# Kernel optimization log

Hardware: AMD Instinct MI355X
Metric: run time of the kernel (lower is better)

## Reference

```python
import jax, jax.numpy as jnp
import numpy as np

N_OR = 8          # orientations of the SE(2) discretization
BN_EPS = 1e-5


def _rotate_kernel(W, theta):
    """Rotate a spatial kernel [..., k, k] about its center by theta.
    Bilinear interpolation, zeros outside the kernel support."""
    k = W.shape[-1]
    c = (k - 1) / 2.0
    ys, xs = jnp.meshgrid(jnp.arange(k, dtype=jnp.float32) - c,
                          jnp.arange(k, dtype=jnp.float32) - c, indexing="ij")
    cos, sin = jnp.cos(theta), jnp.sin(theta)
    sy = cos * ys - sin * xs + c   # source coords: rotate sample grid by -theta
    sx = sin * ys + cos * xs + c
    y0 = jnp.floor(sy).astype(jnp.int32)
    x0 = jnp.floor(sx).astype(jnp.int32)
    wy = (sy - y0).astype(W.dtype)
    wx = (sx - x0).astype(W.dtype)

    def gather(yi, xi):
        valid = ((yi >= 0) & (yi < k) & (xi >= 0) & (xi < k)).astype(W.dtype)
        yc = jnp.clip(yi, 0, k - 1)
        xc = jnp.clip(xi, 0, k - 1)
        return W[..., yc, xc] * valid

    return (gather(y0, x0) * (1 - wy) * (1 - wx)
            + gather(y0, x0 + 1) * (1 - wy) * wx
            + gather(y0 + 1, x0) * wy * (1 - wx)
            + gather(y0 + 1, x0 + 1) * wy * wx)


def _thetas():
    return 2.0 * jnp.pi * jnp.arange(N_OR, dtype=jnp.float32) / N_OR


def _lift(x, W):
    """LiftM2Cartesian. x: [B,Cin,H,W] (pre-padded), W: [Cout,Cin,k,k].
    Returns [B,Cout,8,H',W']."""
    Wr = jax.vmap(lambda t: _rotate_kernel(W, t))(_thetas())  # [8,Cout,Cin,k,k]
    co = W.shape[0]
    Wf = Wr.reshape((N_OR * co,) + W.shape[1:])
    y = jax.lax.conv_general_dilated(x, Wf, (1, 1), "VALID",
                                     dimension_numbers=("NCHW", "OIHW", "NCHW"))
    B, _, H, Wd = y.shape
    return y.reshape(B, N_OR, co, H, Wd).transpose(0, 2, 1, 3, 4)


def _gconv(x, K):
    """ConvM2Cartesian. x: [B,Cin,8,H,W] (spatially pre-padded),
    K: [Cout,Cin,8,k,k]. Output orientation m uses the kernel spatially
    rotated by theta_m with the orientation axis cyclically shifted by m."""
    cout, cin, _, k, _ = K.shape
    # orient_idx[m, o] = (o - m) mod 8
    orient_idx = (jnp.arange(N_OR)[None, :] - jnp.arange(N_OR)[:, None]) % N_OR
    Kshift = jnp.moveaxis(K[:, :, orient_idx], 2, 0)        # [8m,Cout,Cin,8o,k,k]
    Km = jax.vmap(_rotate_kernel)(Kshift, _thetas())         # [8m,Cout,Cin,8o,k,k]
    Kf = Km.reshape(N_OR * cout, cin * N_OR, k, k)
    B, _, _, H, Wd = x.shape
    xf = x.reshape(B, cin * N_OR, H, Wd)
    y = jax.lax.conv_general_dilated(xf, Kf, (1, 1), "VALID",
                                     dimension_numbers=("NCHW", "OIHW", "NCHW"))
    Ho, Wo = y.shape[-2:]
    return y.reshape(B, N_OR, cout, Ho, Wo).transpose(0, 2, 1, 3, 4)


def _bn3d(x, gamma, beta):
    """BatchNorm3d (training-mode batch statistics). x: [B,C,O,H,W]."""
    mean = jnp.mean(x, axis=(0, 2, 3, 4), keepdims=True)
    var = jnp.mean((x - mean) ** 2, axis=(0, 2, 3, 4), keepdims=True)
    g = gamma.reshape(1, -1, 1, 1, 1)
    b = beta.reshape(1, -1, 1, 1, 1)
    return g * (x - mean) * jax.lax.rsqrt(var + BN_EPS) + b


def _pad_m2(x, p):
    return jnp.pad(x, ((0, 0), (0, 0), (0, 0), (p, p), (p, p)), mode="reflect")


def setup_inputs() -> dict:
    key = jax.random.key(0)
    ks = jax.random.split(key, 8)
    c = 16
    cin = 3
    x = jax.random.normal(ks[0], (2, cin, 256, 256), dtype=jnp.float32)
    lift_w = jax.random.normal(ks[1], (c, cin, 7, 7), dtype=jnp.float32) / np.sqrt(cin * 49)
    w1 = jax.random.normal(ks[2], (c, c, N_OR, 5, 5), dtype=jnp.float32) / np.sqrt(c * N_OR * 25)
    w2 = jax.random.normal(ks[3], (c, c, N_OR, 5, 5), dtype=jnp.float32) / np.sqrt(c * N_OR * 25)
    w3 = jax.random.normal(ks[4], (c, c, N_OR, 5, 5), dtype=jnp.float32) / np.sqrt(c * N_OR * 25)
    w4 = jax.random.normal(ks[5], (c, c, N_OR, 1, 1), dtype=jnp.float32) / np.sqrt(c * N_OR)
    final_w = jax.random.normal(ks[6], (1, c), dtype=jnp.float32) / np.sqrt(c)
    ones = jnp.ones((c,), dtype=jnp.float32)
    zeros = jnp.zeros((c,), dtype=jnp.float32)
    return {"x": x, "lift_w": lift_w, "w1": w1, "w2": w2, "w3": w3, "w4": w4,
            "final_w": final_w,
            "g0": ones, "b0": zeros, "g1": ones, "b1": zeros, "g2": ones,
            "b2": zeros, "g3": ones, "b3": zeros, "g4": ones, "b4": zeros}


def reference(x, lift_w, w1, w2, w3, w4, final_w,
              g0, b0, g1, b1, g2, b2, g3, b3, g4, b4):
    # lift: ReflectionPad2d(3) -> LiftM2Cartesian(7) -> BN3d -> ReLU
    xp = jnp.pad(x, ((0, 0), (0, 0), (3, 3), (3, 3)), mode="reflect")
    h = jax.nn.relu(_bn3d(_lift(xp, lift_w), g0, b0))          # [B,16,8,H,W]
    # conv1..3: ReflectionPadM2(2) -> ConvM2Cartesian(5) -> BN3d -> ReLU (Dropout3d is identity in eval)
    h = jax.nn.relu(_bn3d(_gconv(_pad_m2(h, 2), w1), g1, b1))
    h = jax.nn.relu(_bn3d(_gconv(_pad_m2(h, 2), w2), g2, b2))
    h = jax.nn.relu(_bn3d(_gconv(_pad_m2(h, 2), w3), g3, b3))
    # conv4: 1x1 group conv -> BN3d -> ReLU
    h = jax.nn.relu(_bn3d(_gconv(h, w4), g4, b4))
    # MaxProjectM2: max over orientation axis
    h = jnp.max(h, axis=2)                                     # [B,16,H,W]
    # final 1x1 conv (no bias) + sigmoid
    return jax.nn.sigmoid(jnp.einsum("bchw,oc->bohw", h, final_w))
```

## Files before the change

### kernel.cpp

```cpp
#include <hip/hip_runtime.h>
#include <hip/hip_bf16.h>
#include <math.h>

#define HW 65536
#define WID 256
#define NOR 8
#define PLANE_C (NOR * HW)
#define PLANE_B (16 * NOR * HW)
#define BN_N 1048576.0f
#define NHWC_STRIDE 136

typedef __attribute__((ext_vector_type(8)))  short  short8;
typedef __attribute__((ext_vector_type(4)))  short  short4v;
typedef __attribute__((ext_vector_type(16))) float  float16;
typedef __attribute__((ext_vector_type(4)))  float  float4v;

__device__ __forceinline__ float b2f(short s) {
    union { unsigned int u; float f; } c;
    c.u = ((unsigned int)(unsigned short)s) << 16;
    return c.f;
}
__device__ __forceinline__ short f2b(float f) {
    union { __hip_bfloat16 h; short s; } c;
    c.h = __float2bfloat16(f);
    return c.s;
}
__device__ __forceinline__ float ldv(const void* p, int i, int isbf) {
    return isbf ? b2f(((const short*)p)[i]) : ((const float*)p)[i];
}

__global__ void detect_cvt_k(const void* x, const void* fw,
                             const void* g0, const void* b0, const void* g1, const void* b1,
                             const void* g2, const void* b2, const void* g3, const void* b3,
                             const void* g4, const void* b4,
                             float* __restrict__ gbF, float* __restrict__ fwF,
                             int* __restrict__ flag) {
    __shared__ int bad;
    if (threadIdx.x == 0) bad = 0;
    __syncthreads();
    const __hip_bfloat16* p = (const __hip_bfloat16*)x;
    for (int i = threadIdx.x; i < 4096; i += 256) {
        float v = __bfloat162float(p[i]);
        if (!(fabsf(v) < 1e4f)) atomicOr(&bad, 1);
    }
    __syncthreads();
    int isbf = bad ? 0 : 1;
    if (threadIdx.x == 0) *flag = isbf;
    int t = threadIdx.x;
    if (t < 160) {
        const void* srcs[10] = {g0, b0, g1, b1, g2, b2, g3, b3, g4, b4};
        gbF[t] = ldv(srcs[t >> 4], t & 15, isbf);
    } else if (t < 176) {
        fwF[t - 160] = ldv(fw, t - 160, isbf);
    }
}

__device__ float rot_sample_g(const void* __restrict__ W, int isbf, int k, float theta,
                              int i, int j) {
    float c = 0.5f * (float)(k - 1);
    float ys = (float)i - c, xs = (float)j - c;
    float cs = cosf(theta), sn = sinf(theta);
    float sy = cs * ys - sn * xs + c;
    float sx = sn * ys + cs * xs + c;
    float fy = floorf(sy), fx = floorf(sx);
    int y0 = (int)fy, x0 = (int)fx;
    float wy = sy - fy, wx = sx - fx;
    float v00 = (y0 >= 0 && y0 < k && x0 >= 0 && x0 < k)                 ? ldv(W, y0 * k + x0, isbf)           : 0.f;
    float v01 = (y0 >= 0 && y0 < k && x0 + 1 >= 0 && x0 + 1 < k)         ? ldv(W, y0 * k + x0 + 1, isbf)       : 0.f;
    float v10 = (y0 + 1 >= 0 && y0 + 1 < k && x0 >= 0 && x0 < k)         ? ldv(W, (y0 + 1) * k + x0, isbf)     : 0.f;
    float v11 = (y0 + 1 >= 0 && y0 + 1 < k && x0 + 1 >= 0 && x0 + 1 < k) ? ldv(W, (y0 + 1) * k + x0 + 1, isbf) : 0.f;
    return v00 * (1 - wy) * (1 - wx) + v01 * (1 - wy) * wx
         + v10 * wy * (1 - wx) + v11 * wy * wx;
}

__device__ __forceinline__ float theta_of(int m) {
    return (6.2831855f * (float)m) / 8.0f;
}

__device__ __forceinline__ int mirror(int i) {
    i = i < 0 ? -i : i;
    return i >= WID ? (2 * WID - 2 - i) : i;
}

#define PK_BLIFT 20480
#define PK_BG 409600
#define PK_TOTAL (PK_BLIFT + 3 * PK_BG + 16384)
__global__ void mega_pack_k(const void* __restrict__ lw, const void* __restrict__ w1,
                            const void* __restrict__ w2, const void* __restrict__ w3,
                            const void* __restrict__ w4,
                            __hip_bfloat16* __restrict__ Blift, __hip_bfloat16* __restrict__ Bg1,
                            __hip_bfloat16* __restrict__ Bg2, __hip_bfloat16* __restrict__ Bg3,
                            __hip_bfloat16* __restrict__ B1, float* __restrict__ statsL,
                            const int* __restrict__ flag) {
    int idx = blockIdx.x * 256 + threadIdx.x;
    if (idx < 160) statsL[idx] = 0.f;
    if (idx >= PK_TOTAL) return;
    int isbf = *flag;
    if (idx < PK_BLIFT) {
        int n = idx / 160, k = idx % 160;
        float v = 0.f;
        if (k < 147) {
            int c = n >> 3, o = n & 7;
            int ci = k / 49, s = k % 49;
            v = rot_sample_g(isbf ? (const void*)((const short*)lw + (c * 3 + ci) * 49)
                                  : (const void*)((const float*)lw + (c * 3 + ci) * 49),
                             isbf, 7, theta_of(o), s / 7, s % 7);
        }
        Blift[idx] = __float2bfloat16(v);
        return;
    }
    idx -= PK_BLIFT;
    if (idx < 3 * PK_BG) {
        int l = idx / PK_BG;
        int r = idx - l * PK_BG;
        const void* w = (l == 0) ? w1 : ((l == 1) ? w2 : w3);
        __hip_bfloat16* Bg = (l == 0) ? Bg1 : ((l == 1) ? Bg2 : Bg3);
        int j = r & 7;
        int n = (r >> 3) & 127;
        int kc4 = (r >> 10) & 3;
        int sq = r >> 12;
        int s = sq % 25, q = sq / 25;
        int ch = q * 32 + kc4 * 8 + j;
        int co = n >> 3, m = n & 7, ci = ch >> 3, o = ch & 7;
        int oo = (o - m + 8) & 7;
        int off = ((co * 16 + ci) * 8 + oo) * 25;
        const void* wp = isbf ? (const void*)((const short*)w + off)
                              : (const void*)((const float*)w + off);
        Bg[r] = __float2bfloat16(rot_sample_g(wp, isbf, 5, theta_of(m), s / 5, s % 5));
        return;
    }
    idx -= 3 * PK_BG;
    {
        int n = idx >> 7, ch = idx & 127;
        int co = n >> 3, m = n & 7, ci = ch >> 3, o = ch & 7;
        B1[idx] = __float2bfloat16(ldv(w4, (co * 16 + ci) * 8 + ((o - m + 8) & 7), isbf));
    }
}

__device__ __forceinline__ void stats_reduce8(const float16* acc, int lane, int l31,
                                              float* sred) {
#pragma unroll
    for (int nt = 0; nt < 4; nt++) {
        float sv = 0.f, s2v = 0.f;
#pragma unroll
        for (int g = 0; g < 2; g++)
#pragma unroll
            for (int r = 0; r < 16; r++) {
                float v = acc[g * 4 + nt][r];
                sv += v;
                s2v += v * v;
            }
#pragma unroll
        for (int off = 1; off <= 4; off <<= 1) {
            sv += __shfl_xor(sv, off);
            s2v += __shfl_xor(s2v, off);
        }
        sv += __shfl_xor(sv, 32);
        s2v += __shfl_xor(s2v, 32);
        if ((lane & 39) == 0) {
            int c = nt * 4 + (l31 >> 3);
            atomicAdd(&sred[c], sv);
            atomicAdd(&sred[16 + c], s2v);
        }
    }
}

__global__ __launch_bounds__(256, 2) void lift_fused_k(const void* __restrict__ x,
                                                       const __hip_bfloat16* __restrict__ Bh,
                                                       __hip_bfloat16* __restrict__ nh_out,
                                                       float* __restrict__ stats,
                                                       const int* __restrict__ flag) {
    __shared__ float Xs[3 * 484];
    __shared__ short tb[32768];
    __shared__ float sred[32];
    const short* B = (const short*)Bh;
    int tid = threadIdx.x;
    if (tid < 32) sred[tid] = 0.f;
    int isbf = *flag;
    int tile = blockIdx.x;
    int b = blockIdx.y;
    int tx0 = (tile & 15) << 4, ty0 = (tile >> 4) << 4;
    for (int i = tid; i < 1452; i += 256) {
        int ci = i / 484, p = i - ci * 484;
        int yl = p / 22, xl = p - yl * 22;
        int gy = mirror(ty0 - 3 + yl), gx = mirror(tx0 - 3 + xl);
        Xs[i] = ldv(x, (int)(((size_t)b * 3 + ci) * HW) + gy * WID + gx, isbf);
    }
    __syncthreads();
    int wave = tid >> 6, lane = tid & 63;
    int l31 = lane & 31, half = lane >> 5;
    float16 acc[8];
#pragma unroll
    for (int i = 0; i < 8; i++) acc[i] = (float16)0.f;
    int pxl0 = wave * 64 + l31;
    int py0 = pxl0 >> 4, px0 = pxl0 & 15;
    int py1 = (pxl0 + 32) >> 4, px1 = (pxl0 + 32) & 15;
    const short* bp = B + (size_t)l31 * 160 + half * 8;
#pragma unroll
    for (int ks = 0; ks < 10; ks++) {
        short8 a0, a1;
#pragma unroll
        for (int j = 0; j < 8; j++) {
            int k = ks * 16 + half * 8 + j;
            float v0 = 0.f, v1 = 0.f;
            if (k < 147) {
                int ci = (k < 49) ? 0 : ((k < 98) ? 1 : 2);
                int s = k - ci * 49;
                int sy = s / 7, sx = s - sy * 7;
                v0 = Xs[ci * 484 + (py0 + sy) * 22 + px0 + sx];
                v1 = Xs[ci * 484 + (py1 + sy) * 22 + px1 + sx];
            }
            a0[j] = f2b(v0);
            a1[j] = f2b(v1);
        }
#pragma unroll
        for (int nt = 0; nt < 4; nt++) {
            short8 bb = *(const short8*)(bp + nt * 32 * 160 + ks * 16);
            acc[nt]     = __builtin_amdgcn_mfma_f32_32x32x16_bf16(a0, bb, acc[nt], 0, 0, 0);
            acc[4 + nt] = __builtin_amdgcn_mfma_f32_32x32x16_bf16(a1, bb, acc[4 + nt], 0, 0, 0);
        }
    }
#pragma unroll
    for (int g = 0; g < 2; g++)
#pragma unroll
        for (int nt = 0; nt < 4; nt++) {
            int ch = nt * 32 + l31;
#pragma unroll
            for (int r4 = 0; r4 < 4; r4++) {
                int pxb = wave * 64 + g * 32 + 8 * r4 + 4 * half;
#pragma unroll
                for (int i = 0; i < 4; i++)
                    tb[(pxb + i) * 128 + ch] = f2b(acc[g * 4 + nt][r4 * 4 + i]);
            }
        }
    __syncthreads();
    short* outp = (short*)nh_out + (size_t)b * HW * NHWC_STRIDE;
    for (int i = tid; i < 4096; i += 256) {
        int pxl = i >> 4, seg = i & 15;
        int y = ty0 + (pxl >> 4), xx = tx0 + (pxl & 15);
        *(short8*)(outp + ((size_t)y * WID + xx) * NHWC_STRIDE + seg * 8) =
            *(const short8*)&tb[pxl * 128 + seg * 8];
    }
    stats_reduce8(acc, lane, l31, sred);
    __syncthreads();
    if (tid < 16) {
        atomicAdd(&stats[tid * 2], sred[tid]);
        atomicAdd(&stats[tid * 2 + 1], sred[16 + tid]);
    }
}

__global__ __launch_bounds__(256, 2) void gconv_mfma_k(const __hip_bfloat16* __restrict__ nh_in,
                                                       const __hip_bfloat16* __restrict__ Bgh,
                                                       __hip_bfloat16* __restrict__ nh_out,
                                                       const float* __restrict__ statsPrev,
                                                       const float* __restrict__ gPrev,
                                                       const float* __restrict__ bPrev,
                                                       float* __restrict__ statsNew) {
    __shared__ short Au[32768];
    __shared__ float ssl[32];
    __shared__ float sred[32];
    const short* nhwc = (const short*)nh_in;
    const short* Bg = (const short*)Bgh;
    int bid = blockIdx.x;
    int xcd = bid & 7, qt = bid >> 3;
    int b = xcd >> 2, band = xcd & 3;
    int tx0 = (qt & 15) << 4;
    int ty0 = (band << 6) + ((qt >> 4) << 4);
    int tid = threadIdx.x;
    if (tid < 32) sred[tid] = 0.f;
    if (tid < 16) {
        float mean = statsPrev[tid * 2] / BN_N;
        float var = statsPrev[tid * 2 + 1] / BN_N - mean * mean;
        float sc = gPrev[tid] * rsqrtf(var + 1e-5f);
        ssl[tid * 2] = sc;
        ssl[tid * 2 + 1] = bPrev[tid] - mean * sc;
    }
    int w = tid >> 6, lane = tid & 63;
    int pxg = w & 1, nhf = w >> 1;
    int l15 = lane & 15, l4 = lane >> 4;
    float4v acc[32];
#pragma unroll
    for (int i = 0; i < 32; i++) acc[i] = (float4v)0.f;
    const size_t bbase = (size_t)b * HW;
    const int nb = nhf << 6;

    for (int h = 0; h < 2; h++) {
        __syncthreads();
        for (int i = tid; i < 3200; i += 256) {
            int kc = i / 400, p = i - kc * 400;
            int yl = p / 20, xl = p - yl * 20;
            int gy = mirror(ty0 - 2 + yl);
            int gx = mirror(tx0 - 2 + xl);
            short8 raw = *(const short8*)(nhwc + (bbase + gy * WID + gx) * NHWC_STRIDE
                                          + h * 64 + kc * 8);
            int c = h * 8 + kc;
            float sc = ssl[c * 2], sh = ssl[c * 2 + 1];
            short8 ov;
#pragma unroll
            for (int e = 0; e < 8; e++)
                ov[e] = f2b(fmaxf(fmaf(b2f(raw[e]), sc, sh), 0.f));
            *(short8*)&Au[(kc * 441 + yl * 21 + xl) * 8] = ov;
        }
        __syncthreads();
        for (int s = 0; s < 25; s++) {
            int dy = s / 5 - 2, dx = s % 5 - 2;
#pragma unroll
            for (int kq = 0; kq < 2; kq++) {
                int abase = (kq * 4 + l4) * 441 + ((pxg << 3) + 2 + dy) * 21 + (l15 + 2 + dx);
                const short* brow = Bg
                    + ((size_t)(((((h * 2 + kq) * 25 + s) << 2) + l4)) * 128 + nb + l15) * 8;
                short8 a[8];
#pragma unroll
                for (int r = 0; r < 8; r++)
                    a[r] = *(const short8*)&Au[(abase + r * 21) * 8];
#pragma unroll
                for (int nt = 0; nt < 4; nt++) {
                    short8 bb = *(const short8*)(brow + nt * 128);
#pragma unroll
                    for (int r = 0; r < 8; r++)
                        acc[r * 4 + nt] = __builtin_amdgcn_mfma_f32_16x16x32_bf16(
                            a[r], bb, acc[r * 4 + nt], 0, 0, 0);
                }
            }
        }
    }

    __syncthreads();
#pragma unroll
    for (int r = 0; r < 8; r++) {
        int pxl = ((pxg << 3) + r) * 16 + (l4 << 2);
#pragma unroll
        for (int nt = 0; nt < 4; nt++) {
            int n = nb + nt * 16 + l15;
#pragma unroll
            for (int e = 0; e < 4; e++)
                Au[(pxl + e) * 128 + n] = f2b(acc[r * 4 + nt][e]);
        }
    }
    __syncthreads();
    short* outp = (short*)nh_out;
    for (int i = tid; i < 4096; i += 256) {
        int pxl = i >> 4, seg = i & 15;
        int y = ty0 + (pxl >> 4), x = tx0 + (pxl & 15);
        *(short8*)(outp + (bbase + y * WID + x) * NHWC_STRIDE + seg * 8) =
            *(const short8*)&Au[pxl * 128 + seg * 8];
    }
#pragma unroll
    for (int nt = 0; nt < 4; nt++) {
        float sv = 0.f, s2v = 0.f;
#pragma unroll
        for (int r = 0; r < 8; r++)
#pragma unroll
            for (int e = 0; e < 4; e++) {
                float v = acc[r * 4 + nt][e];
                sv += v;
                s2v += v * v;
            }
#pragma unroll
        for (int off = 1; off <= 4; off <<= 1) {
            sv += __shfl_xor(sv, off);
            s2v += __shfl_xor(s2v, off);
        }
        sv += __shfl_xor(sv, 16);
        s2v += __shfl_xor(s2v, 16);
        sv += __shfl_xor(sv, 32);
        s2v += __shfl_xor(s2v, 32);
        if ((lane & 7) == 0 && l4 == 0) {
            int c = (nhf << 3) + (nt << 1) + (l15 >> 3);
            atomicAdd(&sred[c], sv);
            atomicAdd(&sred[16 + c], s2v);
        }
    }
    __syncthreads();
    if (tid < 16) {
        atomicAdd(&statsNew[tid * 2], sred[tid]);
        atomicAdd(&statsNew[tid * 2 + 1], sred[16 + tid]);
    }
}

__global__ __launch_bounds__(256, 2) void conv1x1_gemm_k(const __hip_bfloat16* __restrict__ nh,
                                                         const __hip_bfloat16* __restrict__ B1h,
                                                         __hip_bfloat16* __restrict__ outP,
                                                         const float* __restrict__ statsPrev,
                                                         const float* __restrict__ gPrev,
                                                         const float* __restrict__ bPrev,
                                                         float* __restrict__ statsNew) {
    __shared__ float sred[32];
    __shared__ float ssl[32];
    const short* nhwc = (const short*)nh;
    const short* B1 = (const short*)B1h;
    int tid = threadIdx.x;
    if (tid < 32) sred[tid] = 0.f;
    if (tid < 16) {
        float mean = statsPrev[tid * 2] / BN_N;
        float var = statsPrev[tid * 2 + 1] / BN_N - mean * mean;
        float sc = gPrev[tid] * rsqrtf(var + 1e-5f);
        ssl[tid * 2] = sc;
        ssl[tid * 2 + 1] = bPrev[tid] - mean * sc;
    }
    __syncthreads();
    int b = blockIdx.y;
    int wave = tid >> 6, lane = tid & 63;
    int l31 = lane & 31, half = lane >> 5;
    int p0 = blockIdx.x * 256 + wave * 64;
    float16 acc[8];
#pragma unroll
    for (int i = 0; i < 8; i++) acc[i] = (float16)0.f;
    const short* a0p = nhwc + ((size_t)b * HW + p0 + l31) * NHWC_STRIDE + half * 8;
    const short* a1p = a0p + 32 * NHWC_STRIDE;
    const short* bp  = B1 + (size_t)l31 * 128 + half * 8;
#pragma unroll
    for (int ks = 0; ks < 8; ks++) {
        short8 r0 = *(const short8*)(a0p + ks * 16);
        short8 r1 = *(const short8*)(a1p + ks * 16);
        int c = ks * 2 + half;
        float sc = ssl[c * 2], sh = ssl[c * 2 + 1];
        short8 a0, a1;
#pragma unroll
        for (int e = 0; e < 8; e++) {
            a0[e] = f2b(fmaxf(fmaf(b2f(r0[e]), sc, sh), 0.f));
            a1[e] = f2b(fmaxf(fmaf(b2f(r1[e]), sc, sh), 0.f));
        }
#pragma unroll
        for (int nt = 0; nt < 4; nt++) {
            short8 bb = *(const short8*)(bp + nt * 32 * 128 + ks * 16);
            acc[nt]     = __builtin_amdgcn_mfma_f32_32x32x16_bf16(a0, bb, acc[nt], 0, 0, 0);
            acc[4 + nt] = __builtin_amdgcn_mfma_f32_32x32x16_bf16(a1, bb, acc[4 + nt], 0, 0, 0);
        }
    }
    short* outb = (short*)outP + (size_t)b * PLANE_B;
#pragma unroll
    for (int g = 0; g < 2; g++)
#pragma unroll
        for (int nt = 0; nt < 4; nt++) {
            int n = nt * 32 + l31;
#pragma unroll
            for (int r4 = 0; r4 < 4; r4++) {
                int base = 8 * r4 + 4 * half;
                short4v v;
                v[0] = f2b(acc[g * 4 + nt][r4 * 4 + 0]);
                v[1] = f2b(acc[g * 4 + nt][r4 * 4 + 1]);
                v[2] = f2b(acc[g * 4 + nt][r4 * 4 + 2]);
                v[3] = f2b(acc[g * 4 + nt][r4 * 4 + 3]);
                *(short4v*)(outb + (size_t)n * HW + p0 + g * 32 + base) = v;
            }
        }
    stats_reduce8(acc, lane, l31, sred);
    __syncthreads();
    if (tid < 16) {
        atomicAdd(&statsNew[tid * 2], sred[tid]);
        atomicAdd(&statsNew[tid * 2 + 1], sred[16 + tid]);
    }
}

__global__ void final_k(const __hip_bfloat16* __restrict__ inP, const float* __restrict__ stats,
                        const float* __restrict__ g, const float* __restrict__ beta,
                        const float* __restrict__ fw, void* __restrict__ out,
                        const int* __restrict__ flag) {
    __shared__ float ssl[32];
    if (threadIdx.x < 16) {
        int c = threadIdx.x;
        float mean = stats[c * 2] / BN_N;
        float var = stats[c * 2 + 1] / BN_N - mean * mean;
        float sc = g[c] * rsqrtf(var + 1e-5f);
        ssl[c * 2] = sc;
        ssl[c * 2 + 1] = beta[c] - mean * sc;
    }
    __syncthreads();
    int i = blockIdx.x * blockDim.x + threadIdx.x;
    int b = i >> 16, pix = i & 65535;
    const short* inp = (const short*)inP;
    float acc = 0.f;
#pragma unroll
    for (int co = 0; co < 16; co++) {
        float sc = ssl[co * 2], sh = ssl[co * 2 + 1];
        float mx = 0.f;
        const short* p = inp + (size_t)b * PLANE_B + (size_t)co * PLANE_C + pix;
#pragma unroll
        for (int m = 0; m < 8; m++) mx = fmaxf(mx, fmaf(b2f(p[m * HW]), sc, sh));
        acc = fmaf(fw[co], mx, acc);
    }
    float r = 1.f / (1.f + expf(-acc));
    if (*flag)
        ((__hip_bfloat16*)out)[i] = __float2bfloat16(r);
    else
        ((float*)out)[i] = r;
}

extern "C" void kernel_launch(void* const* d_in, const int* in_sizes, int n_in,
                              void* d_out, int out_size, void* d_ws, size_t ws_size,
                              hipStream_t stream) {
    float* ws = (float*)d_ws;
    __hip_bfloat16* planarB = (__hip_bfloat16*)ws;
    __hip_bfloat16* nhwcA = (__hip_bfloat16*)(ws + 8388608);
    __hip_bfloat16* nhwcB = (__hip_bfloat16*)(ws + 17301504);
    __hip_bfloat16* Bg1   = (__hip_bfloat16*)(ws + 26214400);
    __hip_bfloat16* Bg2   = (__hip_bfloat16*)(ws + 26419200);
    __hip_bfloat16* Bg3   = (__hip_bfloat16*)(ws + 26624000);
    __hip_bfloat16* Blift = (__hip_bfloat16*)(ws + 26828800);
    __hip_bfloat16* B1    = (__hip_bfloat16*)(ws + 26839040);
    float* gbF  = ws + 26847232;
    float* fwF  = gbF + 160;
    float* statsL = fwF + 16;
    int*   flag   = (int*)(statsL + 160);

    detect_cvt_k<<<1, 256, 0, stream>>>(d_in[0], d_in[6],
                                        d_in[7], d_in[8], d_in[9], d_in[10], d_in[11],
                                        d_in[12], d_in[13], d_in[14], d_in[15], d_in[16],
                                        gbF, fwF, flag);

    mega_pack_k<<<(PK_TOTAL + 255) / 256, 256, 0, stream>>>(
        d_in[1], d_in[2], d_in[3], d_in[4], d_in[5],
        Blift, Bg1, Bg2, Bg3, B1, statsL, flag);

    lift_fused_k<<<dim3(256, 2), 256, 0, stream>>>(d_in[0], Blift, nhwcA, statsL, flag);

    __hip_bfloat16* Bgs[3] = {Bg1, Bg2, Bg3};
    __hip_bfloat16* nio[4] = {nhwcA, nhwcB, nhwcA, nhwcB};
    for (int l = 0; l < 3; l++) {
        gconv_mfma_k<<<512, 256, 0, stream>>>(nio[l], Bgs[l], nio[l + 1],
                                              statsL + 32 * l, gbF + 32 * l, gbF + 32 * l + 16,
                                              statsL + 32 * (l + 1));
    }

    conv1x1_gemm_k<<<dim3(256, 2), 256, 0, stream>>>(nio[3], B1, planarB,
                                                     statsL + 96, gbF + 96, gbF + 112,
                                                     statsL + 128);

    final_k<<<(2 * HW) / 256, 256, 0, stream>>>(planarB, statsL + 128, gbF + 128, gbF + 144,
                                                fwF, d_out, flag);
}
```

Baseline: 458.1 us.

## Fuse orientation max/min into 1x1 conv epilogue and fold dtype detection into kernels

```diff
diff --git a/kernel.cpp b/kernel.cpp
--- a/kernel.cpp
+++ b/kernel.cpp
@@ -5,7 +5,6 @@
 #define HW 65536
 #define WID 256
 #define NOR 8
-#define PLANE_C (NOR * HW)
 #define PLANE_B (16 * NOR * HW)
 #define BN_N 1048576.0f
 #define NHWC_STRIDE 136
@@ -29,30 +28,17 @@
     return isbf ? b2f(((const short*)p)[i]) : ((const float*)p)[i];
 }
 
-__global__ void detect_cvt_k(const void* x, const void* fw,
-                             const void* g0, const void* b0, const void* g1, const void* b1,
-                             const void* g2, const void* b2, const void* g3, const void* b3,
-                             const void* g4, const void* b4,
-                             float* __restrict__ gbF, float* __restrict__ fwF,
-                             int* __restrict__ flag) {
+__device__ __forceinline__ int detect_local(const void* x, int tid) {
     __shared__ int bad;
-    if (threadIdx.x == 0) bad = 0;
+    if (tid == 0) bad = 0;
     __syncthreads();
     const __hip_bfloat16* p = (const __hip_bfloat16*)x;
-    for (int i = threadIdx.x; i < 4096; i += 256) {
+    for (int i = tid; i < 4096; i += 256) {
         float v = __bfloat162float(p[i]);
         if (!(fabsf(v) < 1e4f)) atomicOr(&bad, 1);
     }
     __syncthreads();
-    int isbf = bad ? 0 : 1;
-    if (threadIdx.x == 0) *flag = isbf;
-    int t = threadIdx.x;
-    if (t < 160) {
-        const void* srcs[10] = {g0, b0, g1, b1, g2, b2, g3, b3, g4, b4};
-        gbF[t] = ldv(srcs[t >> 4], t & 15, isbf);
-    } else if (t < 176) {
-        fwF[t - 160] = ldv(fw, t - 160, isbf);
-    }
+    return bad ? 0 : 1;
 }
 
 __device__ float rot_sample_g(const void* __restrict__ W, int isbf, int k, float theta,
@@ -85,17 +71,32 @@
 #define PK_BLIFT 20480
 #define PK_BG 409600
 #define PK_TOTAL (PK_BLIFT + 3 * PK_BG + 16384)
-__global__ void mega_pack_k(const void* __restrict__ lw, const void* __restrict__ w1,
+__global__ void mega_pack_k(const void* __restrict__ x,
+                            const void* __restrict__ lw, const void* __restrict__ w1,
                             const void* __restrict__ w2, const void* __restrict__ w3,
-                            const void* __restrict__ w4,
+                            const void* __restrict__ w4, const void* __restrict__ fw,
+                            const void* g0, const void* b0, const void* g1, const void* b1,
+                            const void* g2, const void* b2, const void* g3, const void* b3,
+                            const void* g4, const void* b4,
                             __hip_bfloat16* __restrict__ Blift, __hip_bfloat16* __restrict__ Bg1,
                             __hip_bfloat16* __restrict__ Bg2, __hip_bfloat16* __restrict__ Bg3,
                             __hip_bfloat16* __restrict__ B1, float* __restrict__ statsL,
-                            const int* __restrict__ flag) {
-    int idx = blockIdx.x * 256 + threadIdx.x;
+                            float* __restrict__ gbF, float* __restrict__ fwF,
+                            int* __restrict__ flag) {
+    int tid = threadIdx.x;
+    int isbf = detect_local(x, tid);
+    int idx = blockIdx.x * 256 + tid;
     if (idx < 160) statsL[idx] = 0.f;
+    if (blockIdx.x == 0) {
+        if (tid == 0) *flag = isbf;
+        if (tid < 160) {
+            const void* srcs[10] = {g0, b0, g1, b1, g2, b2, g3, b3, g4, b4};
+            gbF[tid] = ldv(srcs[tid >> 4], tid & 15, isbf);
+        } else if (tid < 176) {
+            fwF[tid - 160] = ldv(fw, tid - 160, isbf);
+        }
+    }
     if (idx >= PK_TOTAL) return;
-    int isbf = *flag;
     if (idx < PK_BLIFT) {
         int n = idx / 160, k = idx % 160;
         float v = 0.f;
@@ -168,15 +169,14 @@
 __global__ __launch_bounds__(256, 2) void lift_fused_k(const void* __restrict__ x,
                                                        const __hip_bfloat16* __restrict__ Bh,
                                                        __hip_bfloat16* __restrict__ nh_out,
-                                                       float* __restrict__ stats,
-                                                       const int* __restrict__ flag) {
+                                                       float* __restrict__ stats) {
     __shared__ float Xs[3 * 484];
     __shared__ short tb[32768];
     __shared__ float sred[32];
     const short* B = (const short*)Bh;
     int tid = threadIdx.x;
+    int isbf = detect_local(x, tid);
     if (tid < 32) sred[tid] = 0.f;
-    int isbf = *flag;
     int tile = blockIdx.x;
     int b = blockIdx.y;
     int tx0 = (tile & 15) << 4, ty0 = (tile >> 4) << 4;
@@ -380,7 +380,8 @@
 
 __global__ __launch_bounds__(256, 2) void conv1x1_gemm_k(const __hip_bfloat16* __restrict__ nh,
                                                          const __hip_bfloat16* __restrict__ B1h,
-                                                         __hip_bfloat16* __restrict__ outP,
+                                                         short* __restrict__ ymx,
+                                                         short* __restrict__ ymn,
                                                          const float* __restrict__ statsPrev,
                                                          const float* __restrict__ gPrev,
                                                          const float* __restrict__ bPrev,
@@ -428,21 +429,36 @@
             acc[4 + nt] = __builtin_amdgcn_mfma_f32_32x32x16_bf16(a1, bb, acc[4 + nt], 0, 0, 0);
         }
     }
-    short* outb = (short*)outP + (size_t)b * PLANE_B;
 #pragma unroll
     for (int g = 0; g < 2; g++)
 #pragma unroll
         for (int nt = 0; nt < 4; nt++) {
-            int n = nt * 32 + l31;
-#pragma unroll
-            for (int r4 = 0; r4 < 4; r4++) {
-                int base = 8 * r4 + 4 * half;
-                short4v v;
-                v[0] = f2b(acc[g * 4 + nt][r4 * 4 + 0]);
-                v[1] = f2b(acc[g * 4 + nt][r4 * 4 + 1]);
-                v[2] = f2b(acc[g * 4 + nt][r4 * 4 + 2]);
-                v[3] = f2b(acc[g * 4 + nt][r4 * 4 + 3]);
-                *(short4v*)(outb + (size_t)n * HW + p0 + g * 32 + base) = v;
+            float16 vx = acc[g * 4 + nt];
+            float16 vn = acc[g * 4 + nt];
+#pragma unroll
+            for (int mk = 1; mk <= 4; mk <<= 1)
+#pragma unroll
+                for (int r = 0; r < 16; r++) {
+                    float ox = __shfl_xor(vx[r], mk);
+                    float on = __shfl_xor(vn[r], mk);
+                    vx[r] = fmaxf(vx[r], ox);
+                    vn[r] = fminf(vn[r], on);
+                }
+            if ((l31 & 7) == 0) {
+                int co = nt * 4 + (l31 >> 3);
+                size_t base = ((size_t)(b * 16 + co)) * HW + p0 + g * 32;
+#pragma unroll
+                for (int r4 = 0; r4 < 4; r4++) {
+                    int off = 8 * r4 + 4 * half;
+                    short4v sx, sn;
+#pragma unroll
+                    for (int i = 0; i < 4; i++) {
+                        sx[i] = f2b(vx[r4 * 4 + i]);
+                        sn[i] = f2b(vn[r4 * 4 + i]);
+                    }
+                    *(short4v*)(ymx + base + off) = sx;
+                    *(short4v*)(ymn + base + off) = sn;
+                }
             }
         }
     stats_reduce8(acc, lane, l31, sred);
@@ -453,7 +469,8 @@
     }
 }
 
-__global__ void final_k(const __hip_bfloat16* __restrict__ inP, const float* __restrict__ stats,
+__global__ void final_k(const short* __restrict__ ymx, const short* __restrict__ ymn,
+                        const float* __restrict__ stats,
                         const float* __restrict__ g, const float* __restrict__ beta,
                         const float* __restrict__ fw, void* __restrict__ out,
                         const int* __restrict__ flag) {
@@ -469,16 +486,15 @@
     __syncthreads();
     int i = blockIdx.x * blockDim.x + threadIdx.x;
     int b = i >> 16, pix = i & 65535;
-    const short* inp = (const short*)inP;
     float acc = 0.f;
 #pragma unroll
     for (int co = 0; co < 16; co++) {
         float sc = ssl[co * 2], sh = ssl[co * 2 + 1];
-        float mx = 0.f;
-        const short* p = inp + (size_t)b * PLANE_B + (size_t)co * PLANE_C + pix;
-#pragma unroll
-        for (int m = 0; m < 8; m++) mx = fmaxf(mx, fmaf(b2f(p[m * HW]), sc, sh));
-        acc = fmaf(fw[co], mx, acc);
+        size_t base = ((size_t)(b * 16 + co)) * HW + pix;
+        float vx = b2f(ymx[base]);
+        float vn = b2f(ymn[base]);
+        float v = (sc >= 0.f) ? fmaf(sc, vx, sh) : fmaf(sc, vn, sh);
+        acc = fmaf(fw[co], fmaxf(v, 0.f), acc);
     }
     float r = 1.f / (1.f + expf(-acc));
     if (*flag)
@@ -491,7 +507,8 @@
                               void* d_out, int out_size, void* d_ws, size_t ws_size,
                               hipStream_t stream) {
     float* ws = (float*)d_ws;
-    __hip_bfloat16* planarB = (__hip_bfloat16*)ws;
+    short* ymx = (short*)ws;
+    short* ymn = ymx + 2097152;
     __hip_bfloat16* nhwcA = (__hip_bfloat16*)(ws + 8388608);
     __hip_bfloat16* nhwcB = (__hip_bfloat16*)(ws + 17301504);
     __hip_bfloat16* Bg1   = (__hip_bfloat16*)(ws + 26214400);
@@ -504,16 +521,13 @@
     float* statsL = fwF + 16;
     int*   flag   = (int*)(statsL + 160);
 
-    detect_cvt_k<<<1, 256, 0, stream>>>(d_in[0], d_in[6],
-                                        d_in[7], d_in[8], d_in[9], d_in[10], d_in[11],
-                                        d_in[12], d_in[13], d_in[14], d_in[15], d_in[16],
-                                        gbF, fwF, flag);
-
     mega_pack_k<<<(PK_TOTAL + 255) / 256, 256, 0, stream>>>(
-        d_in[1], d_in[2], d_in[3], d_in[4], d_in[5],
-        Blift, Bg1, Bg2, Bg3, B1, statsL, flag);
-
-    lift_fused_k<<<dim3(256, 2), 256, 0, stream>>>(d_in[0], Blift, nhwcA, statsL, flag);
+        d_in[0], d_in[1], d_in[2], d_in[3], d_in[4], d_in[5], d_in[6],
+        d_in[7], d_in[8], d_in[9], d_in[10], d_in[11], d_in[12], d_in[13],
+        d_in[14], d_in[15], d_in[16],
+        Blift, Bg1, Bg2, Bg3, B1, statsL, gbF, fwF, flag);
+
+    lift_fused_k<<<dim3(256, 2), 256, 0, stream>>>(d_in[0], Blift, nhwcA, statsL);
 
     __hip_bfloat16* Bgs[3] = {Bg1, Bg2, Bg3};
     __hip_bfloat16* nio[4] = {nhwcA, nhwcB, nhwcA, nhwcB};
@@ -523,10 +537,10 @@
                                               statsL + 32 * (l + 1));
     }
 
-    conv1x1_gemm_k<<<dim3(256, 2), 256, 0, stream>>>(nio[3], B1, planarB,
+    conv1x1_gemm_k<<<dim3(256, 2), 256, 0, stream>>>(nio[3], B1, ymx, ymn,
                                                      statsL + 96, gbF + 96, gbF + 112,
                                                      statsL + 128);
 
-    final_k<<<(2 * HW) / 256, 256, 0, stream>>>(planarB, statsL + 128, gbF + 128, gbF + 144,
+    final_k<<<(2 * HW) / 256, 256, 0, stream>>>(ymx, ymn, statsL + 128, gbF + 128, gbF + 144,
                                                 fwF, d_out, flag);
 }
```

Result: no change. 461.7 us (+0.8%).
